# Performance work log

Measured on AMD Instinct MI355X. Metric: run time of the kernel, lower is better.

## Reference

```python
import jax, jax.numpy as jnp
import numpy as np

B, H, W, DIM, NH, HD = 2, 64, 160, 256, 8, 32
R0, R1 = 1, 1                      # win_r (x, y)
WX, WY = 2 * R0 + 2, 2 * R1 + 2    # window extents
A = WX * WY                        # attn_num = 16
SCALE = HD ** (-0.5)


def setup_inputs() -> dict:
    key = jax.random.key(0)
    ks = jax.random.split(key, 6)
    x = jax.random.normal(ks[0], (B, H, W, DIM), jnp.float32)
    # float match positions anywhere in the image; clamp in reference() keeps windows in-bounds
    u = jax.random.uniform(ks[1], (B, H * W, 2), jnp.float32)
    max_offset = u * jnp.array([W, H], jnp.float32)
    Wq = jax.random.normal(ks[2], (DIM, NH * HD), jnp.float32) * 0.02
    Wk = jax.random.normal(ks[3], (DIM, NH * HD), jnp.float32) * 0.02
    Wv = jax.random.normal(ks[4], (DIM, NH * HD), jnp.float32) * 0.02
    Wproj = jax.random.normal(ks[5], (NH * HD, DIM), jnp.float32) * 0.02
    return dict(x=x, max_offset=max_offset, Wq=Wq, Wk=Wk, Wv=Wv, Wproj=Wproj)


def reference(x, max_offset, Wq, Wk, Wv, Wproj):
    b, h, w, _ = x.shape
    n = h * w
    xf = x.reshape(b, n, -1)
    q = (xf @ Wq).reshape(b, n, NH, HD)
    k = (xf @ Wk).reshape(b, n, NH, HD)
    v = (xf @ Wv).reshape(b, n, NH, HD)

    # clamp_max_offset: keep the (2r+2)^2 window fully inside the image
    ox = jnp.clip(max_offset[..., 0], R0, w - 1 - R0 - 0.001)
    oy = jnp.clip(max_offset[..., 1], R1, h - 1 - R1 - 0.001)
    mx, my = jnp.floor(ox), jnp.floor(oy)
    fx, fy = ox - mx, oy - my  # bilinear fractions

    # window gather indices: rows my-R1..my+R1+1, cols mx-R0..mx+R0+1
    ix = mx.astype(jnp.int32)[..., None] + jnp.arange(-R0, R0 + 2)  # (b,n,WX)
    iy = my.astype(jnp.int32)[..., None] + jnp.arange(-R1, R1 + 2)  # (b,n,WY)
    idx = (iy[:, :, :, None] * w + ix[:, :, None, :]).reshape(b, n, A)  # (b,n,A)

    gather = jax.vmap(lambda t, i: t[i])  # per-batch row gather
    kg = gather(k.reshape(b, n, NH * HD), idx).reshape(b, n, A, NH, HD)
    vg = gather(v.reshape(b, n, NH * HD), idx).reshape(b, n, A, NH, HD)

    attn = jnp.einsum('bnhd,bnahd->bnha', q, kg) * SCALE  # (b,n,NH,A)

    # bilinear weights: edge elements weighted by (1-f)/f, interior by 1
    wx = jnp.concatenate([(1 - fx)[..., None], jnp.ones((b, n, 2 * R0), fx.dtype), fx[..., None]], axis=-1)
    wy = jnp.concatenate([(1 - fy)[..., None], jnp.ones((b, n, 2 * R1), fy.dtype), fy[..., None]], axis=-1)
    bw = (wy[:, :, :, None] * wx[:, :, None, :]).reshape(b, n, 1, A)

    # bilinear-weighted stable softmax
    m = jnp.max(attn, axis=-1, keepdims=True)
    e = jnp.exp(attn - m) * bw
    p = e / jnp.sum(e, axis=-1, keepdims=True)

    out = jnp.einsum('bnha,bnahd->bnhd', p, vg).reshape(b, n, NH * HD)
    out = out @ Wproj
    return out.reshape(b, h, w, -1)
```

## Files before the change

### kernel.cpp

```cpp
#include <hip/hip_runtime.h>
#include <math.h>

#define Bb   2
#define Hh   64
#define Ww   160
#define DIMc 256
#define Nn   (Hh * Ww)
#define NPOS (Bb * Nn)
#define SCALEf 0.17677669529663687f

typedef unsigned short u16;
typedef unsigned int   u32;
typedef __bf16 bf16x8 __attribute__((ext_vector_type(8)));
typedef float  f32x4  __attribute__((ext_vector_type(4)));

__device__ __forceinline__ u16 f2bf(float f) {
    u32 u = __float_as_uint(f);
    u += 0x7fffu + ((u >> 16) & 1u);
    return (u16)(u >> 16);
}
__device__ __forceinline__ u32 pack2(float lo, float hi) {
    return (u32)f2bf(lo) | ((u32)f2bf(hi) << 16);
}
__device__ __forceinline__ float bflo(u32 u) { return __uint_as_float(u << 16); }
__device__ __forceinline__ float bfhi(u32 u) { return __uint_as_float(u & 0xffff0000u); }

__device__ __forceinline__ void gload16(const void* g, void* l) {
    __builtin_amdgcn_global_load_lds(
        (const __attribute__((address_space(1))) unsigned int*)g,
        (__attribute__((address_space(3))) unsigned int*)l,
        16, 0, 0);
}

__global__ __launch_bounds__(256) void prep_w(const float* __restrict__ Wq,
                                              const float* __restrict__ Wk,
                                              const float* __restrict__ Wv,
                                              const float* __restrict__ Wp,
                                              u16* __restrict__ WtAll)
{
    int id = blockIdx.x * 256 + threadIdx.x;
    int wsel = id >> 16;
    int rem  = id & 65535;
    int kk = rem >> 8, nn = rem & 255;
    const float* W = (wsel == 0) ? Wq : (wsel == 1) ? Wk : (wsel == 2) ? Wv : Wp;
    WtAll[(size_t)wsel * 65536 + nn * 256 + kk] = f2bf(W[kk * 256 + nn]);
}

__global__ __launch_bounds__(256) void gemm_qkv(const float* __restrict__ x,
                                                const u16* __restrict__ WtAll,
                                                u16* __restrict__ q,
                                                u16* __restrict__ k,
                                                u16* __restrict__ v)
{
    __shared__ __align__(16) char smem[32768];
    u16* sA = (u16*)smem;
    u16* sB = (u16*)(smem + 8192);

    const int z = blockIdx.z;
    u16* Cb = (z == 0) ? q : (z == 1) ? k : v;
    const u16* Btg = WtAll + (size_t)z * 65536;

    const int t    = threadIdx.x;
    const int lane = t & 63;
    const int wv   = t >> 6;
    const int wm   = wv & 1;
    const int wn   = wv >> 1;
    const int m0   = blockIdx.y * 128;
    const int n0   = blockIdx.x * 128;

    const int r0  = t >> 2;
    const int kc0 = (t & 3) * 8;

    const int col  = lane & 15;
    const int quad = lane >> 4;

    f32x4 acc[4][4];
#pragma unroll
    for (int i = 0; i < 4; ++i)
#pragma unroll
        for (int j = 0; j < 4; ++j)
            acc[i][j] = (f32x4){0.f, 0.f, 0.f, 0.f};

    const u16* Bbase = Btg + (size_t)n0 * 256;
    char* ldsB0 = smem + 8192 + wv * 1024;
    char* ldsB1 = smem + 8192 + 4096 + wv * 1024;

    for (int k0 = 0; k0 < 256; k0 += 32) {
        const float* ap0 = x + (size_t)(m0 + r0) * 256 + k0 + kc0;
        const float* ap1 = x + (size_t)(m0 + 64 + r0) * 256 + k0 + kc0;
        float4 f0 = *(const float4*)ap0, f1 = *(const float4*)(ap0 + 4);
        float4 f2 = *(const float4*)ap1, f3 = *(const float4*)(ap1 + 4);
        uint4 a0, a1;
        a0.x = pack2(f0.x, f0.y); a0.y = pack2(f0.z, f0.w);
        a0.z = pack2(f1.x, f1.y); a0.w = pack2(f1.z, f1.w);
        a1.x = pack2(f2.x, f2.y); a1.y = pack2(f2.z, f2.w);
        a1.z = pack2(f3.x, f3.y); a1.w = pack2(f3.z, f3.w);

        __syncthreads();
        *(uint4*)(sA + r0 * 32 + kc0)        = a0;
        *(uint4*)(sA + (64 + r0) * 32 + kc0) = a1;
        gload16(Bbase + (size_t)r0        * 256 + k0 + kc0, ldsB0);
        gload16(Bbase + (size_t)(64 + r0) * 256 + k0 + kc0, ldsB1);
        __syncthreads();

        bf16x8 af[4], bfr[4];
#pragma unroll
        for (int mt = 0; mt < 4; ++mt)
            af[mt] = *(const bf16x8*)(sA + (wm * 64 + mt * 16 + col) * 32 + quad * 8);
#pragma unroll
        for (int nt = 0; nt < 4; ++nt)
            bfr[nt] = *(const bf16x8*)(sB + (wn * 64 + nt * 16 + col) * 32 + quad * 8);

#pragma unroll
        for (int mt = 0; mt < 4; ++mt)
#pragma unroll
            for (int nt = 0; nt < 4; ++nt)
                acc[mt][nt] = __builtin_amdgcn_mfma_f32_16x16x32_bf16(af[mt], bfr[nt], acc[mt][nt], 0, 0, 0);
    }

    __syncthreads();
    u16* sC = (u16*)smem;
#pragma unroll
    for (int mt = 0; mt < 4; ++mt)
#pragma unroll
        for (int nt = 0; nt < 4; ++nt) {
            const int rw = wm * 64 + mt * 16 + quad * 4;
            const int cl = wn * 64 + nt * 16 + col;
#pragma unroll
            for (int rr = 0; rr < 4; ++rr)
                sC[(rw + rr) * 128 + cl] = f2bf(acc[mt][nt][rr]);
        }
    __syncthreads();
#pragma unroll
    for (int i = 0; i < 8; ++i) {
        int j   = i * 256 + t;
        int row = j >> 4;
        int off = (j & 15) * 8;
        int cg  = (n0 >> 3) + (j & 15);
        int dst = (z == 2) ? cg * 8 : ((cg & 3) * 64 + (cg >> 2) * 8);
        *(uint4*)(Cb + (size_t)(m0 + row) * 256 + dst) = *(const uint4*)(sC + row * 128 + off);
    }
}

__global__ __launch_bounds__(256) void attn_kernel(const u16* __restrict__ q,
                                                   const u16* __restrict__ k,
                                                   const u16* __restrict__ v,
                                                   const float* __restrict__ moff,
                                                   u16* __restrict__ ao)
{
    const int wv   = threadIdx.x >> 6;
    const int lane = threadIdx.x & 63;
    const int pos  = blockIdx.x * 4 + wv;
    const int rowbase = (pos >= Nn) ? Nn : 0;

    float2 mo = *(const float2*)(moff + (size_t)pos * 2);
    float ox = fminf(fmaxf(mo.x, 1.0f), (float)(Ww - 2) - 0.001f);
    float oy = fminf(fmaxf(mo.y, 1.0f), (float)(Hh - 2) - 0.001f);
    float mxf = floorf(ox), myf = floorf(oy);
    float fx = ox - mxf, fy = oy - myf;
    int imx = (int)mxf, imy = (int)myf;

    const int h  = lane & 7;
    const int a0 = lane >> 3;

    uint4 q4[4];
    {
        const u16* qp = q + (size_t)pos * 256 + h * 8;
#pragma unroll
        for (int jj = 0; jj < 4; ++jj) q4[jj] = *(const uint4*)(qp + jj * 64);
    }

    float s[2];
#pragma unroll
    for (int p = 0; p < 2; ++p) {
        int a   = a0 + 8 * p;
        int row = rowbase + (imy + (a >> 2) - 1) * Ww + imx + (a & 3) - 1;
        const u16* kp = k + (size_t)row * 256 + h * 8;
        float acc = 0.f;
#pragma unroll
        for (int jj = 0; jj < 4; ++jj) {
            uint4 kw = *(const uint4*)(kp + jj * 64);
            acc += bflo(q4[jj].x) * bflo(kw.x) + bfhi(q4[jj].x) * bfhi(kw.x)
                 + bflo(q4[jj].y) * bflo(kw.y) + bfhi(q4[jj].y) * bfhi(kw.y)
                 + bflo(q4[jj].z) * bflo(kw.z) + bfhi(q4[jj].z) * bfhi(kw.z)
                 + bflo(q4[jj].w) * bflo(kw.w) + bfhi(q4[jj].w) * bfhi(kw.w);
        }
        s[p] = acc * SCALEf;
    }

    auto wc = [](int r, float f) { return r == 0 ? 1.f - f : (r == 3 ? f : 1.f); };
    float bw0 = wc(a0 >> 2, fy) * wc(a0 & 3, fx);
    float bw1 = wc((a0 + 8) >> 2, fy) * wc(a0 & 3, fx);

    float m = fmaxf(s[0], s[1]);
    m = fmaxf(m, __shfl_xor(m, 8));
    m = fmaxf(m, __shfl_xor(m, 16));
    m = fmaxf(m, __shfl_xor(m, 32));
    float e0 = expf(s[0] - m) * bw0;
    float e1 = expf(s[1] - m) * bw1;
    float sum = e0 + e1;
    sum += __shfl_xor(sum, 8);
    sum += __shfl_xor(sum, 16);
    sum += __shfl_xor(sum, 32);
    float inv = 1.f / sum;
    float p0 = e0 * inv, p1 = e1 * inv;

    float acc0 = 0.f, acc1 = 0.f, acc2 = 0.f, acc3 = 0.f;
    const int myh = lane >> 3;
#pragma unroll
    for (int a = 0; a < 16; ++a) {
        int row = rowbase + (imy + (a >> 2) - 1) * Ww + imx + (a & 3) - 1;
        uint2 vw = *(const uint2*)(v + (size_t)row * 256 + 4 * lane);
        int src = ((a & 7) << 3) | myh;
        float pa = __shfl(a < 8 ? p0 : p1, src);
        acc0 += pa * bflo(vw.x); acc1 += pa * bfhi(vw.x);
        acc2 += pa * bflo(vw.y); acc3 += pa * bfhi(vw.y);
    }
    uint2 o;
    o.x = pack2(acc0, acc1);
    o.y = pack2(acc2, acc3);
    *(uint2*)(ao + (size_t)pos * 256 + 4 * lane) = o;
}

__global__ __launch_bounds__(256) void gemm_proj(const u16* __restrict__ Ab,
                                                 const u16* __restrict__ Btg,
                                                 float* __restrict__ Cf)
{
    __shared__ __align__(16) char smem[32768];
    u16* sA = (u16*)smem;
    u16* sB = (u16*)(smem + 8192);

    const int t    = threadIdx.x;
    const int lane = t & 63;
    const int wv   = t >> 6;
    const int wm   = wv & 1;
    const int wn   = wv >> 1;
    const int m0   = blockIdx.y * 128;
    const int n0   = blockIdx.x * 128;

    const int r0  = t >> 2;
    const int kc0 = (t & 3) * 8;

    const int col  = lane & 15;
    const int quad = lane >> 4;

    f32x4 acc[4][4];
#pragma unroll
    for (int i = 0; i < 4; ++i)
#pragma unroll
        for (int j = 0; j < 4; ++j)
            acc[i][j] = (f32x4){0.f, 0.f, 0.f, 0.f};

    const u16* Bbase = Btg + (size_t)n0 * 256;
    char* ldsA0 = smem + wv * 1024;
    char* ldsA1 = smem + 4096 + wv * 1024;
    char* ldsB0 = smem + 8192 + wv * 1024;
    char* ldsB1 = smem + 8192 + 4096 + wv * 1024;

    for (int k0 = 0; k0 < 256; k0 += 32) {
        __syncthreads();
        gload16(Ab    + (size_t)(m0 + r0)      * 256 + k0 + kc0, ldsA0);
        gload16(Ab    + (size_t)(m0 + 64 + r0) * 256 + k0 + kc0, ldsA1);
        gload16(Bbase + (size_t)r0             * 256 + k0 + kc0, ldsB0);
        gload16(Bbase + (size_t)(64 + r0)      * 256 + k0 + kc0, ldsB1);
        __syncthreads();

        bf16x8 af[4], bfr[4];
#pragma unroll
        for (int mt = 0; mt < 4; ++mt)
            af[mt] = *(const bf16x8*)(sA + (wm * 64 + mt * 16 + col) * 32 + quad * 8);
#pragma unroll
        for (int nt = 0; nt < 4; ++nt)
            bfr[nt] = *(const bf16x8*)(sB + (wn * 64 + nt * 16 + col) * 32 + quad * 8);

#pragma unroll
        for (int mt = 0; mt < 4; ++mt)
#pragma unroll
            for (int nt = 0; nt < 4; ++nt)
                acc[mt][nt] = __builtin_amdgcn_mfma_f32_16x16x32_bf16(af[mt], bfr[nt], acc[mt][nt], 0, 0, 0);
    }

    __syncthreads();
    float* sC = (float*)smem;
#pragma unroll
    for (int ph = 0; ph < 2; ++ph) {
        if (wm == ph) {
#pragma unroll
            for (int mt = 0; mt < 4; ++mt)
#pragma unroll
                for (int nt = 0; nt < 4; ++nt) {
                    const int rw = mt * 16 + quad * 4;
                    const int cl = wn * 64 + nt * 16 + col;
#pragma unroll
                    for (int rr = 0; rr < 4; ++rr)
                        sC[(rw + rr) * 128 + cl] = acc[mt][nt][rr];
                }
        }
        __syncthreads();
#pragma unroll
        for (int i = 0; i < 8; ++i) {
            int j   = i * 256 + t;
            int row = j >> 5;
            int off = (j & 31) * 4;
            *(float4*)(Cf + (size_t)(m0 + ph * 64 + row) * 256 + n0 + off) =
                *(const float4*)(sC + row * 128 + off);
        }
        __syncthreads();
    }
}

extern "C" void kernel_launch(void* const* d_in, const int* in_sizes, int n_in,
                              void* d_out, int out_size, void* d_ws, size_t ws_size,
                              hipStream_t stream)
{
    const float* x     = (const float*)d_in[0];
    const float* moff  = (const float*)d_in[1];
    const float* Wq    = (const float*)d_in[2];
    const float* Wk    = (const float*)d_in[3];
    const float* Wv    = (const float*)d_in[4];
    const float* Wproj = (const float*)d_in[5];
    float* out = (float*)d_out;

    const size_t NTOT = (size_t)Bb * Nn * DIMc;
    u16* ws    = (u16*)d_ws;
    u16* WtAll = ws;
    u16* q     = WtAll + 4 * 65536;
    u16* k     = q + NTOT;
    u16* v     = k + NTOT;
    u16* ao    = v + NTOT;

    prep_w<<<dim3(1024), dim3(256), 0, stream>>>(Wq, Wk, Wv, Wproj, WtAll);
    gemm_qkv<<<dim3(2, 160, 3), dim3(256), 0, stream>>>(x, WtAll, q, k, v);
    attn_kernel<<<dim3(NPOS / 4), dim3(256), 0, stream>>>(q, k, v, moff, ao);
    gemm_proj<<<dim3(2, 160, 1), dim3(256), 0, stream>>>(ao, WtAll + (size_t)3 * 65536, out);
}
```

Before: 149.3 us.

## Use natural head-major Q/K layout and restructure window attention lane mapping

The QKV GEMM epilogue no longer permutes Q/K columns into an interleaved layout; it writes them in natural head-major order. The attention kernel now maps each lane to (head, 8-element chunk, parity of window slot). Each lane loads one contiguous 16-byte piece of its head's Q and K per window slot, and the partial dot products are reduced across 4 lanes with shuffles. Each lane then holds 8 scores and does most of the softmax max and sum in registers, replacing the earlier cross-lane reductions. The aim is more contiguous K reads and fewer shuffles, at the cost of more registers and extra shuffles in the dot-product reduction.

```diff
diff --git a/kernel.cpp b/kernel.cpp
--- a/kernel.cpp
+++ b/kernel.cpp
@@ -136,9 +136,7 @@
         int j   = i * 256 + t;
         int row = j >> 4;
         int off = (j & 15) * 8;
-        int cg  = (n0 >> 3) + (j & 15);
-        int dst = (z == 2) ? cg * 8 : ((cg & 3) * 64 + (cg >> 2) * 8);
-        *(uint4*)(Cb + (size_t)(m0 + row) * 256 + dst) = *(const uint4*)(sC + row * 128 + off);
+        *(uint4*)(Cb + (size_t)(m0 + row) * 256 + n0 + off) = *(const uint4*)(sC + row * 128 + off);
     }
 }
 
@@ -160,59 +158,54 @@
     float fx = ox - mxf, fy = oy - myf;
     int imx = (int)mxf, imy = (int)myf;
 
-    const int h  = lane & 7;
-    const int a0 = lane >> 3;
-
-    uint4 q4[4];
-    {
-        const u16* qp = q + (size_t)pos * 256 + h * 8;
-#pragma unroll
-        for (int jj = 0; jj < 4; ++jj) q4[jj] = *(const uint4*)(qp + jj * 64);
-    }
-
-    float s[2];
-#pragma unroll
-    for (int p = 0; p < 2; ++p) {
-        int a   = a0 + 8 * p;
+    const int hi = lane >> 5;
+    const int h  = (lane >> 2) & 7;
+    const int jj = lane & 3;
+
+    const uint4 q4 = *(const uint4*)(q + (size_t)pos * 256 + h * 32 + jj * 8);
+
+    float s[8];
+#pragma unroll
+    for (int i = 0; i < 8; ++i) {
+        int a   = 2 * i + hi;
         int row = rowbase + (imy + (a >> 2) - 1) * Ww + imx + (a & 3) - 1;
-        const u16* kp = k + (size_t)row * 256 + h * 8;
-        float acc = 0.f;
-#pragma unroll
-        for (int jj = 0; jj < 4; ++jj) {
-            uint4 kw = *(const uint4*)(kp + jj * 64);
-            acc += bflo(q4[jj].x) * bflo(kw.x) + bfhi(q4[jj].x) * bfhi(kw.x)
-                 + bflo(q4[jj].y) * bflo(kw.y) + bfhi(q4[jj].y) * bfhi(kw.y)
-                 + bflo(q4[jj].z) * bflo(kw.z) + bfhi(q4[jj].z) * bfhi(kw.z)
-                 + bflo(q4[jj].w) * bflo(kw.w) + bfhi(q4[jj].w) * bfhi(kw.w);
-        }
-        s[p] = acc * SCALEf;
+        uint4 kw = *(const uint4*)(k + (size_t)row * 256 + h * 32 + jj * 8);
+        float acc = bflo(q4.x) * bflo(kw.x) + bfhi(q4.x) * bfhi(kw.x)
+                  + bflo(q4.y) * bflo(kw.y) + bfhi(q4.y) * bfhi(kw.y)
+                  + bflo(q4.z) * bflo(kw.z) + bfhi(q4.z) * bfhi(kw.z)
+                  + bflo(q4.w) * bflo(kw.w) + bfhi(q4.w) * bfhi(kw.w);
+        acc += __shfl_xor(acc, 1);
+        acc += __shfl_xor(acc, 2);
+        s[i] = acc * SCALEf;
     }
 
     auto wc = [](int r, float f) { return r == 0 ? 1.f - f : (r == 3 ? f : 1.f); };
-    float bw0 = wc(a0 >> 2, fy) * wc(a0 & 3, fx);
-    float bw1 = wc((a0 + 8) >> 2, fy) * wc(a0 & 3, fx);
-
-    float m = fmaxf(s[0], s[1]);
-    m = fmaxf(m, __shfl_xor(m, 8));
-    m = fmaxf(m, __shfl_xor(m, 16));
+    float m = s[0];
+#pragma unroll
+    for (int i = 1; i < 8; ++i) m = fmaxf(m, s[i]);
     m = fmaxf(m, __shfl_xor(m, 32));
-    float e0 = expf(s[0] - m) * bw0;
-    float e1 = expf(s[1] - m) * bw1;
-    float sum = e0 + e1;
-    sum += __shfl_xor(sum, 8);
-    sum += __shfl_xor(sum, 16);
+
+    float p[8];
+    float sum = 0.f;
+#pragma unroll
+    for (int i = 0; i < 8; ++i) {
+        int a = 2 * i + hi;
+        float bwv = wc(a >> 2, fy) * wc(a & 3, fx);
+        p[i] = expf(s[i] - m) * bwv;
+        sum += p[i];
+    }
     sum += __shfl_xor(sum, 32);
     float inv = 1.f / sum;
-    float p0 = e0 * inv, p1 = e1 * inv;
+#pragma unroll
+    for (int i = 0; i < 8; ++i) p[i] *= inv;
 
     float acc0 = 0.f, acc1 = 0.f, acc2 = 0.f, acc3 = 0.f;
-    const int myh = lane >> 3;
+    const int hsel = (lane >> 3) << 2;
 #pragma unroll
     for (int a = 0; a < 16; ++a) {
         int row = rowbase + (imy + (a >> 2) - 1) * Ww + imx + (a & 3) - 1;
         uint2 vw = *(const uint2*)(v + (size_t)row * 256 + 4 * lane);
-        int src = ((a & 7) << 3) | myh;
-        float pa = __shfl(a < 8 ? p0 : p1, src);
+        float pa = __shfl(p[a >> 1], ((a & 1) << 5) + hsel);
         acc0 += pa * bflo(vw.x); acc1 += pa * bfhi(vw.x);
         acc2 += pa * bflo(vw.y); acc3 += pa * bfhi(vw.y);
     }
```

New measurement: 154.9 us. 3.7% more time.

## Store q/k/v in plain head-major layout and process two positions per wave

Applied to the files above, without the earlier changes.

The QKV GEMM epilogue now writes columns in natural order, not in the interleaved layout. The attention kernel reads each head's 32 contiguous dims as four consecutive uint4 loads per lane. Each wave now handles two query positions with interleaved loads, shuffles and softmax, and the grid is halved, to expose more memory-level parallelism for the gathers. This raises register use per thread and produces a different per-lane access pattern for K.

```diff
diff --git a/kernel.cpp b/kernel.cpp
--- a/kernel.cpp
+++ b/kernel.cpp
@@ -136,9 +136,7 @@
         int j   = i * 256 + t;
         int row = j >> 4;
         int off = (j & 15) * 8;
-        int cg  = (n0 >> 3) + (j & 15);
-        int dst = (z == 2) ? cg * 8 : ((cg & 3) * 64 + (cg >> 2) * 8);
-        *(uint4*)(Cb + (size_t)(m0 + row) * 256 + dst) = *(const uint4*)(sC + row * 128 + off);
+        *(uint4*)(Cb + (size_t)(m0 + row) * 256 + n0 + off) = *(const uint4*)(sC + row * 128 + off);
     }
 }
 
@@ -150,76 +148,112 @@
 {
     const int wv   = threadIdx.x >> 6;
     const int lane = threadIdx.x & 63;
-    const int pos  = blockIdx.x * 4 + wv;
-    const int rowbase = (pos >= Nn) ? Nn : 0;
-
-    float2 mo = *(const float2*)(moff + (size_t)pos * 2);
-    float ox = fminf(fmaxf(mo.x, 1.0f), (float)(Ww - 2) - 0.001f);
-    float oy = fminf(fmaxf(mo.y, 1.0f), (float)(Hh - 2) - 0.001f);
-    float mxf = floorf(ox), myf = floorf(oy);
-    float fx = ox - mxf, fy = oy - myf;
-    int imx = (int)mxf, imy = (int)myf;
-
-    const int h  = lane & 7;
-    const int a0 = lane >> 3;
-
-    uint4 q4[4];
-    {
-        const u16* qp = q + (size_t)pos * 256 + h * 8;
-#pragma unroll
-        for (int jj = 0; jj < 4; ++jj) q4[jj] = *(const uint4*)(qp + jj * 64);
-    }
-
-    float s[2];
+    const int h    = lane & 7;
+    const int a0   = lane >> 3;
+    const int myh  = lane >> 3;
+
+    int pos[2], rowbase[2];
+    pos[0] = blockIdx.x * 8 + wv;
+    pos[1] = pos[0] + 4;
+#pragma unroll
+    for (int P = 0; P < 2; ++P) rowbase[P] = (pos[P] >= Nn) ? Nn : 0;
+
+    float fx[2], fy[2];
+    int   imx[2], imy[2];
+#pragma unroll
+    for (int P = 0; P < 2; ++P) {
+        float2 mo = *(const float2*)(moff + (size_t)pos[P] * 2);
+        float ox = fminf(fmaxf(mo.x, 1.0f), (float)(Ww - 2) - 0.001f);
+        float oy = fminf(fmaxf(mo.y, 1.0f), (float)(Hh - 2) - 0.001f);
+        float mxf = floorf(ox), myf = floorf(oy);
+        fx[P] = ox - mxf; fy[P] = oy - myf;
+        imx[P] = (int)mxf; imy[P] = (int)myf;
+    }
+
+    uint4 q4[2][4];
+#pragma unroll
+    for (int P = 0; P < 2; ++P) {
+        const uint4* qp = (const uint4*)(q + (size_t)pos[P] * 256 + h * 32);
+#pragma unroll
+        for (int jj = 0; jj < 4; ++jj) q4[P][jj] = qp[jj];
+    }
+
+    float s[2][2];
 #pragma unroll
     for (int p = 0; p < 2; ++p) {
-        int a   = a0 + 8 * p;
-        int row = rowbase + (imy + (a >> 2) - 1) * Ww + imx + (a & 3) - 1;
-        const u16* kp = k + (size_t)row * 256 + h * 8;
-        float acc = 0.f;
-#pragma unroll
-        for (int jj = 0; jj < 4; ++jj) {
-            uint4 kw = *(const uint4*)(kp + jj * 64);
-            acc += bflo(q4[jj].x) * bflo(kw.x) + bfhi(q4[jj].x) * bfhi(kw.x)
-                 + bflo(q4[jj].y) * bflo(kw.y) + bfhi(q4[jj].y) * bfhi(kw.y)
-                 + bflo(q4[jj].z) * bflo(kw.z) + bfhi(q4[jj].z) * bfhi(kw.z)
-                 + bflo(q4[jj].w) * bflo(kw.w) + bfhi(q4[jj].w) * bfhi(kw.w);
-        }
-        s[p] = acc * SCALEf;
+#pragma unroll
+        for (int P = 0; P < 2; ++P) {
+            int a   = a0 + 8 * p;
+            int row = rowbase[P] + (imy[P] + (a >> 2) - 1) * Ww + imx[P] + (a & 3) - 1;
+            const uint4* kp = (const uint4*)(k + (size_t)row * 256 + h * 32);
+            float acc = 0.f;
+#pragma unroll
+            for (int jj = 0; jj < 4; ++jj) {
+                uint4 kw = kp[jj];
+                acc += bflo(q4[P][jj].x) * bflo(kw.x) + bfhi(q4[P][jj].x) * bfhi(kw.x)
+                     + bflo(q4[P][jj].y) * bflo(kw.y) + bfhi(q4[P][jj].y) * bfhi(kw.y)
+                     + bflo(q4[P][jj].z) * bflo(kw.z) + bfhi(q4[P][jj].z) * bfhi(kw.z)
+                     + bflo(q4[P][jj].w) * bflo(kw.w) + bfhi(q4[P][jj].w) * bfhi(kw.w);
+            }
+            s[P][p] = acc * SCALEf;
+        }
     }
 
     auto wc = [](int r, float f) { return r == 0 ? 1.f - f : (r == 3 ? f : 1.f); };
-    float bw0 = wc(a0 >> 2, fy) * wc(a0 & 3, fx);
-    float bw1 = wc((a0 + 8) >> 2, fy) * wc(a0 & 3, fx);
-
-    float m = fmaxf(s[0], s[1]);
-    m = fmaxf(m, __shfl_xor(m, 8));
-    m = fmaxf(m, __shfl_xor(m, 16));
-    m = fmaxf(m, __shfl_xor(m, 32));
-    float e0 = expf(s[0] - m) * bw0;
-    float e1 = expf(s[1] - m) * bw1;
-    float sum = e0 + e1;
-    sum += __shfl_xor(sum, 8);
-    sum += __shfl_xor(sum, 16);
-    sum += __shfl_xor(sum, 32);
-    float inv = 1.f / sum;
-    float p0 = e0 * inv, p1 = e1 * inv;
-
-    float acc0 = 0.f, acc1 = 0.f, acc2 = 0.f, acc3 = 0.f;
-    const int myh = lane >> 3;
+
+    float m[2], e0[2], e1[2], sum[2];
+#pragma unroll
+    for (int P = 0; P < 2; ++P) m[P] = fmaxf(s[P][0], s[P][1]);
+#pragma unroll
+    for (int P = 0; P < 2; ++P) m[P] = fmaxf(m[P], __shfl_xor(m[P], 8));
+#pragma unroll
+    for (int P = 0; P < 2; ++P) m[P] = fmaxf(m[P], __shfl_xor(m[P], 16));
+#pragma unroll
+    for (int P = 0; P < 2; ++P) m[P] = fmaxf(m[P], __shfl_xor(m[P], 32));
+#pragma unroll
+    for (int P = 0; P < 2; ++P) {
+        float bw0 = wc(a0 >> 2, fy[P]) * wc(a0 & 3, fx[P]);
+        float bw1 = wc((a0 + 8) >> 2, fy[P]) * wc(a0 & 3, fx[P]);
+        e0[P] = expf(s[P][0] - m[P]) * bw0;
+        e1[P] = expf(s[P][1] - m[P]) * bw1;
+        sum[P] = e0[P] + e1[P];
+    }
+#pragma unroll
+    for (int P = 0; P < 2; ++P) sum[P] += __shfl_xor(sum[P], 8);
+#pragma unroll
+    for (int P = 0; P < 2; ++P) sum[P] += __shfl_xor(sum[P], 16);
+#pragma unroll
+    for (int P = 0; P < 2; ++P) sum[P] += __shfl_xor(sum[P], 32);
+
+    float p0[2], p1[2];
+#pragma unroll
+    for (int P = 0; P < 2; ++P) {
+        float inv = 1.f / sum[P];
+        p0[P] = e0[P] * inv;
+        p1[P] = e1[P] * inv;
+    }
+
+    float acc0[2] = {0.f, 0.f}, acc1[2] = {0.f, 0.f};
+    float acc2[2] = {0.f, 0.f}, acc3[2] = {0.f, 0.f};
 #pragma unroll
     for (int a = 0; a < 16; ++a) {
-        int row = rowbase + (imy + (a >> 2) - 1) * Ww + imx + (a & 3) - 1;
-        uint2 vw = *(const uint2*)(v + (size_t)row * 256 + 4 * lane);
         int src = ((a & 7) << 3) | myh;
-        float pa = __shfl(a < 8 ? p0 : p1, src);
-        acc0 += pa * bflo(vw.x); acc1 += pa * bfhi(vw.x);
-        acc2 += pa * bflo(vw.y); acc3 += pa * bfhi(vw.y);
-    }
-    uint2 o;
-    o.x = pack2(acc0, acc1);
-    o.y = pack2(acc2, acc3);
-    *(uint2*)(ao + (size_t)pos * 256 + 4 * lane) = o;
+#pragma unroll
+        for (int P = 0; P < 2; ++P) {
+            int row = rowbase[P] + (imy[P] + (a >> 2) - 1) * Ww + imx[P] + (a & 3) - 1;
+            uint2 vw = *(const uint2*)(v + (size_t)row * 256 + 4 * lane);
+            float pa = __shfl(a < 8 ? p0[P] : p1[P], src);
+            acc0[P] += pa * bflo(vw.x); acc1[P] += pa * bfhi(vw.x);
+            acc2[P] += pa * bflo(vw.y); acc3[P] += pa * bfhi(vw.y);
+        }
+    }
+#pragma unroll
+    for (int P = 0; P < 2; ++P) {
+        uint2 o;
+        o.x = pack2(acc0[P], acc1[P]);
+        o.y = pack2(acc2[P], acc3[P]);
+        *(uint2*)(ao + (size_t)pos[P] * 256 + 4 * lane) = o;
+    }
 }
 
 __global__ __launch_bounds__(256) void gemm_proj(const u16* __restrict__ Ab,
@@ -331,6 +365,6 @@
 
     prep_w<<<dim3(1024), dim3(256), 0, stream>>>(Wq, Wk, Wv, Wproj, WtAll);
     gemm_qkv<<<dim3(2, 160, 3), dim3(256), 0, stream>>>(x, WtAll, q, k, v);
-    attn_kernel<<<dim3(NPOS / 4), dim3(256), 0, stream>>>(q, k, v, moff, ao);
+    attn_kernel<<<dim3(NPOS / 8), dim3(256), 0, stream>>>(q, k, v, moff, ao);
     gemm_proj<<<dim3(2, 160, 1), dim3(256), 0, stream>>>(ao, WtAll + (size_t)3 * 65536, out);
 }
```

Result: no change. 149.9 us (+0.4%).

## Use full-width 64x256 GEMM tiles and a contiguous per-head q/k layout

Applied to the files above, without the earlier changes.

Both GEMMs move from 128x128 output tiles on a 2x2 wave grid to 64-row by 256-column tiles, with each wave covering 64 output columns. Each block now spans the full N dimension, so the fp32 activation x (and ao in the projection) is loaded and converted to bf16 once per row block instead of once per column half. The cost is more weight loads from L2 per block and a different LDS footprint. The interleaved q/k column permutation is dropped in favour of plain row-major output, and the attention kernel now reads each head's 32 contiguous elements per lane.

```diff
diff --git a/kernel.cpp b/kernel.cpp
--- a/kernel.cpp
+++ b/kernel.cpp
@@ -54,7 +54,7 @@
 {
     __shared__ __align__(16) char smem[32768];
     u16* sA = (u16*)smem;
-    u16* sB = (u16*)(smem + 8192);
+    u16* sB = (u16*)(smem + 4096);
 
     const int z = blockIdx.z;
     u16* Cb = (z == 0) ? q : (z == 1) ? k : v;
@@ -63,10 +63,7 @@
     const int t    = threadIdx.x;
     const int lane = t & 63;
     const int wv   = t >> 6;
-    const int wm   = wv & 1;
-    const int wn   = wv >> 1;
-    const int m0   = blockIdx.y * 128;
-    const int n0   = blockIdx.x * 128;
+    const int m0   = blockIdx.y * 64;
 
     const int r0  = t >> 2;
     const int kc0 = (t & 3) * 8;
@@ -81,35 +78,28 @@
         for (int j = 0; j < 4; ++j)
             acc[i][j] = (f32x4){0.f, 0.f, 0.f, 0.f};
 
-    const u16* Bbase = Btg + (size_t)n0 * 256;
-    char* ldsB0 = smem + 8192 + wv * 1024;
-    char* ldsB1 = smem + 8192 + 4096 + wv * 1024;
-
     for (int k0 = 0; k0 < 256; k0 += 32) {
-        const float* ap0 = x + (size_t)(m0 + r0) * 256 + k0 + kc0;
-        const float* ap1 = x + (size_t)(m0 + 64 + r0) * 256 + k0 + kc0;
-        float4 f0 = *(const float4*)ap0, f1 = *(const float4*)(ap0 + 4);
-        float4 f2 = *(const float4*)ap1, f3 = *(const float4*)(ap1 + 4);
-        uint4 a0, a1;
+        const float* ap = x + (size_t)(m0 + r0) * 256 + k0 + kc0;
+        float4 f0 = *(const float4*)ap, f1 = *(const float4*)(ap + 4);
+        uint4 a0;
         a0.x = pack2(f0.x, f0.y); a0.y = pack2(f0.z, f0.w);
         a0.z = pack2(f1.x, f1.y); a0.w = pack2(f1.z, f1.w);
-        a1.x = pack2(f2.x, f2.y); a1.y = pack2(f2.z, f2.w);
-        a1.z = pack2(f3.x, f3.y); a1.w = pack2(f3.z, f3.w);
-
-        __syncthreads();
-        *(uint4*)(sA + r0 * 32 + kc0)        = a0;
-        *(uint4*)(sA + (64 + r0) * 32 + kc0) = a1;
-        gload16(Bbase + (size_t)r0        * 256 + k0 + kc0, ldsB0);
-        gload16(Bbase + (size_t)(64 + r0) * 256 + k0 + kc0, ldsB1);
+
+        __syncthreads();
+        *(uint4*)(sA + r0 * 32 + kc0) = a0;
+        gload16(Btg + (size_t)r0         * 256 + k0 + kc0, smem + 4096  + wv * 1024);
+        gload16(Btg + (size_t)(64 + r0)  * 256 + k0 + kc0, smem + 8192  + wv * 1024);
+        gload16(Btg + (size_t)(128 + r0) * 256 + k0 + kc0, smem + 12288 + wv * 1024);
+        gload16(Btg + (size_t)(192 + r0) * 256 + k0 + kc0, smem + 16384 + wv * 1024);
         __syncthreads();
 
         bf16x8 af[4], bfr[4];
 #pragma unroll
         for (int mt = 0; mt < 4; ++mt)
-            af[mt] = *(const bf16x8*)(sA + (wm * 64 + mt * 16 + col) * 32 + quad * 8);
+            af[mt] = *(const bf16x8*)(sA + (mt * 16 + col) * 32 + quad * 8);
 #pragma unroll
         for (int nt = 0; nt < 4; ++nt)
-            bfr[nt] = *(const bf16x8*)(sB + (wn * 64 + nt * 16 + col) * 32 + quad * 8);
+            bfr[nt] = *(const bf16x8*)(sB + (wv * 64 + nt * 16 + col) * 32 + quad * 8);
 
 #pragma unroll
         for (int mt = 0; mt < 4; ++mt)
@@ -124,21 +114,19 @@
     for (int mt = 0; mt < 4; ++mt)
 #pragma unroll
         for (int nt = 0; nt < 4; ++nt) {
-            const int rw = wm * 64 + mt * 16 + quad * 4;
-            const int cl = wn * 64 + nt * 16 + col;
+            const int rw = mt * 16 + quad * 4;
+            const int cl = wv * 64 + nt * 16 + col;
 #pragma unroll
             for (int rr = 0; rr < 4; ++rr)
-                sC[(rw + rr) * 128 + cl] = f2bf(acc[mt][nt][rr]);
+                sC[(rw + rr) * 256 + cl] = f2bf(acc[mt][nt][rr]);
         }
     __syncthreads();
 #pragma unroll
     for (int i = 0; i < 8; ++i) {
         int j   = i * 256 + t;
-        int row = j >> 4;
-        int off = (j & 15) * 8;
-        int cg  = (n0 >> 3) + (j & 15);
-        int dst = (z == 2) ? cg * 8 : ((cg & 3) * 64 + (cg >> 2) * 8);
-        *(uint4*)(Cb + (size_t)(m0 + row) * 256 + dst) = *(const uint4*)(sC + row * 128 + off);
+        int row = j >> 5;
+        int off = (j & 31) * 8;
+        *(uint4*)(Cb + (size_t)(m0 + row) * 256 + off) = *(const uint4*)(sC + row * 256 + off);
     }
 }
 
@@ -165,9 +153,9 @@
 
     uint4 q4[4];
     {
-        const u16* qp = q + (size_t)pos * 256 + h * 8;
-#pragma unroll
-        for (int jj = 0; jj < 4; ++jj) q4[jj] = *(const uint4*)(qp + jj * 64);
+        const uint4* qp = (const uint4*)(q + (size_t)pos * 256 + h * 32);
+#pragma unroll
+        for (int jj = 0; jj < 4; ++jj) q4[jj] = qp[jj];
     }
 
     float s[2];
@@ -175,11 +163,11 @@
     for (int p = 0; p < 2; ++p) {
         int a   = a0 + 8 * p;
         int row = rowbase + (imy + (a >> 2) - 1) * Ww + imx + (a & 3) - 1;
-        const u16* kp = k + (size_t)row * 256 + h * 8;
+        const uint4* kp = (const uint4*)(k + (size_t)row * 256 + h * 32);
         float acc = 0.f;
 #pragma unroll
         for (int jj = 0; jj < 4; ++jj) {
-            uint4 kw = *(const uint4*)(kp + jj * 64);
+            uint4 kw = kp[jj];
             acc += bflo(q4[jj].x) * bflo(kw.x) + bfhi(q4[jj].x) * bfhi(kw.x)
                  + bflo(q4[jj].y) * bflo(kw.y) + bfhi(q4[jj].y) * bfhi(kw.y)
                  + bflo(q4[jj].z) * bflo(kw.z) + bfhi(q4[jj].z) * bfhi(kw.z)
@@ -228,15 +216,12 @@
 {
     __shared__ __align__(16) char smem[32768];
     u16* sA = (u16*)smem;
-    u16* sB = (u16*)(smem + 8192);
+    u16* sB = (u16*)(smem + 4096);
 
     const int t    = threadIdx.x;
     const int lane = t & 63;
     const int wv   = t >> 6;
-    const int wm   = wv & 1;
-    const int wn   = wv >> 1;
-    const int m0   = blockIdx.y * 128;
-    const int n0   = blockIdx.x * 128;
+    const int m0   = blockIdx.y * 64;
 
     const int r0  = t >> 2;
     const int kc0 = (t & 3) * 8;
@@ -251,27 +236,22 @@
         for (int j = 0; j < 4; ++j)
             acc[i][j] = (f32x4){0.f, 0.f, 0.f, 0.f};
 
-    const u16* Bbase = Btg + (size_t)n0 * 256;
-    char* ldsA0 = smem + wv * 1024;
-    char* ldsA1 = smem + 4096 + wv * 1024;
-    char* ldsB0 = smem + 8192 + wv * 1024;
-    char* ldsB1 = smem + 8192 + 4096 + wv * 1024;
-
     for (int k0 = 0; k0 < 256; k0 += 32) {
         __syncthreads();
-        gload16(Ab    + (size_t)(m0 + r0)      * 256 + k0 + kc0, ldsA0);
-        gload16(Ab    + (size_t)(m0 + 64 + r0) * 256 + k0 + kc0, ldsA1);
-        gload16(Bbase + (size_t)r0             * 256 + k0 + kc0, ldsB0);
-        gload16(Bbase + (size_t)(64 + r0)      * 256 + k0 + kc0, ldsB1);
+        gload16(Ab  + (size_t)(m0 + r0)  * 256 + k0 + kc0, smem          + wv * 1024);
+        gload16(Btg + (size_t)r0         * 256 + k0 + kc0, smem + 4096   + wv * 1024);
+        gload16(Btg + (size_t)(64 + r0)  * 256 + k0 + kc0, smem + 8192   + wv * 1024);
+        gload16(Btg + (size_t)(128 + r0) * 256 + k0 + kc0, smem + 12288  + wv * 1024);
+        gload16(Btg + (size_t)(192 + r0) * 256 + k0 + kc0, smem + 16384  + wv * 1024);
         __syncthreads();
 
         bf16x8 af[4], bfr[4];
 #pragma unroll
         for (int mt = 0; mt < 4; ++mt)
-            af[mt] = *(const bf16x8*)(sA + (wm * 64 + mt * 16 + col) * 32 + quad * 8);
+            af[mt] = *(const bf16x8*)(sA + (mt * 16 + col) * 32 + quad * 8);
 #pragma unroll
         for (int nt = 0; nt < 4; ++nt)
-            bfr[nt] = *(const bf16x8*)(sB + (wn * 64 + nt * 16 + col) * 32 + quad * 8);
+            bfr[nt] = *(const bf16x8*)(sB + (wv * 64 + nt * 16 + col) * 32 + quad * 8);
 
 #pragma unroll
         for (int mt = 0; mt < 4; ++mt)
@@ -284,26 +264,26 @@
     float* sC = (float*)smem;
 #pragma unroll
     for (int ph = 0; ph < 2; ++ph) {
-        if (wm == ph) {
-#pragma unroll
-            for (int mt = 0; mt < 4; ++mt)
-#pragma unroll
-                for (int nt = 0; nt < 4; ++nt) {
-                    const int rw = mt * 16 + quad * 4;
-                    const int cl = wn * 64 + nt * 16 + col;
-#pragma unroll
-                    for (int rr = 0; rr < 4; ++rr)
-                        sC[(rw + rr) * 128 + cl] = acc[mt][nt][rr];
-                }
+#pragma unroll
+        for (int lm = 0; lm < 2; ++lm) {
+            const int mt = 2 * ph + lm;
+#pragma unroll
+            for (int nt = 0; nt < 4; ++nt) {
+                const int rw = lm * 16 + quad * 4;
+                const int cl = wv * 64 + nt * 16 + col;
+#pragma unroll
+                for (int rr = 0; rr < 4; ++rr)
+                    sC[(rw + rr) * 256 + cl] = acc[mt][nt][rr];
+            }
         }
         __syncthreads();
 #pragma unroll
         for (int i = 0; i < 8; ++i) {
             int j   = i * 256 + t;
-            int row = j >> 5;
-            int off = (j & 31) * 4;
-            *(float4*)(Cf + (size_t)(m0 + ph * 64 + row) * 256 + n0 + off) =
-                *(const float4*)(sC + row * 128 + off);
+            int row = j >> 6;
+            int off = (j & 63) * 4;
+            *(float4*)(Cf + (size_t)(m0 + ph * 32 + row) * 256 + off) =
+                *(const float4*)(sC + row * 256 + off);
         }
         __syncthreads();
     }
@@ -330,7 +310,7 @@
     u16* ao    = v + NTOT;
 
     prep_w<<<dim3(1024), dim3(256), 0, stream>>>(Wq, Wk, Wv, Wproj, WtAll);
-    gemm_qkv<<<dim3(2, 160, 3), dim3(256), 0, stream>>>(x, WtAll, q, k, v);
+    gemm_qkv<<<dim3(1, 320, 3), dim3(256), 0, stream>>>(x, WtAll, q, k, v);
     attn_kernel<<<dim3(NPOS / 4), dim3(256), 0, stream>>>(q, k, v, moff, ao);
-    gemm_proj<<<dim3(2, 160, 1), dim3(256), 0, stream>>>(ao, WtAll + (size_t)3 * 65536, out);
-}
+    gemm_proj<<<dim3(1, 320), dim3(256), 0, stream>>>(ao, WtAll + (size_t)3 * 65536, out);
+}
```

After: 143.2 us. 1.04x faster.
